# Optimization experiments

Hardware: AMD Instinct MI355X
Metric: run time of the kernel (lower is better)

The kernel has to match this reference:

```python
import jax, jax.numpy as jnp
import numpy as np

NUM_EMBEDDINGS = 1024
EMBEDDING_DIM = 64
BETA = 0.25  # commitment_cost


def setup_inputs() -> dict:
    key = jax.random.key(0)
    k1, k2 = jax.random.split(key)
    z = jax.random.normal(k1, (32, EMBEDDING_DIM, 32, 32), dtype=jnp.float32)
    embedding = jax.random.normal(k2, (NUM_EMBEDDINGS, EMBEDDING_DIM), dtype=jnp.float32)
    return {"z": z, "embedding": embedding}


def reference(z, embedding):
    B, D, H, W = z.shape
    beta = jnp.asarray(BETA, z.dtype)
    # [B, D, H, W] -> [B*H*W, D]
    z_flat = jnp.transpose(z, (0, 2, 3, 1)).reshape(-1, D)
    # squared L2 distances to each code: ||z||^2 - 2 z.e^T + ||e||^2  -> [N, E]
    dist = (
        jnp.sum(z_flat * z_flat, axis=1, keepdims=True)
        - 2.0 * (z_flat @ embedding.T)
        + jnp.sum(embedding * embedding, axis=1)
    )
    encoding_indices = jnp.argmin(dist, axis=1)  # [N]
    # direct gather instead of one-hot matmul (same math)
    quantized = embedding[encoding_indices]  # [N, D]
    quantized = jnp.transpose(quantized.reshape(B, H, W, D), (0, 3, 1, 2))
    commitment_loss = beta * jnp.mean(
        (jax.lax.stop_gradient(z) - quantized) ** 2
    )
    codebook_loss = jnp.mean((z - jax.lax.stop_gradient(quantized)) ** 2)
    loss = commitment_loss + codebook_loss
    # straight-through estimator
    quantized_st = z + jax.lax.stop_gradient(quantized - z)
    return (quantized_st, loss, encoding_indices)
```

## Files before the change

### kernel.cpp

```cpp
#include <hip/hip_runtime.h>

typedef __attribute__((ext_vector_type(8))) short short8;
typedef __attribute__((ext_vector_type(4))) float f32x4;
typedef unsigned int uint32;

#define QOUT 2097152

__device__ __forceinline__ unsigned short f2bf(float f){
  uint32 u = __float_as_uint(f);
  return (unsigned short)((u + 0x7FFFu + ((u >> 16) & 1u)) >> 16);
}
__device__ __forceinline__ float bf2f(unsigned short h){
  return __uint_as_float(((uint32)h) << 16);
}
__device__ __forceinline__ uint32 med3u(uint32 a, uint32 b, uint32 c){
  uint32 d;
  asm("v_med3_u32 %0, %1, %2, %3" : "=v"(d) : "v"(a), "v"(b), "v"(c));
  return d;
}

__global__ void vq_prep(const float* __restrict__ emb, unsigned char* __restrict__ ebg,
                        float* __restrict__ nrm64, int* __restrict__ cnt){
  int u = blockIdx.x * 256 + threadIdx.x;
  if (u == 0) *cnt = 0;
  int C = u >> 3, oct = u & 7;
  const float4* e4 = reinterpret_cast<const float4*>(emb) + C * 16 + oct * 2;
  float4 v0 = e4[0], v1 = e4[1];
  float vv[8] = {v0.x, v0.y, v0.z, v0.w, v1.x, v1.y, v1.z, v1.w};
  float s = 0.f;
  short8 H, L;
#pragma unroll
  for (int j = 0; j < 8; ++j){
    float v = vv[j];
    s = fmaf(v, v, s);
    unsigned short hs = f2bf(v);
    unsigned short ls = f2bf(v - bf2f(hs));
    H[j] = (short)hs; L[j] = (short)ls;
  }
  int ng = C >> 4, c15 = C & 15, kf = oct >> 2, gg = oct & 3;
  unsigned char* base = ebg + ng * 4096 + kf * 2048 + (gg * 16 + c15) * 16;
  *reinterpret_cast<short8*>(base) = H;
  *reinterpret_cast<short8*>(base + 1024) = L;
#pragma unroll
  for (int d = 1; d < 8; d <<= 1) s += __shfl_xor(s, d);
  if (oct == 0) nrm64[C] = 0.5f * s + 128.0f;
}

__global__ __launch_bounds__(512, 4) void vq_main(
    const float* __restrict__ z, const float* __restrict__ emb,
    const unsigned char* __restrict__ ebg, const float* __restrict__ nrm64,
    float* __restrict__ out, float* __restrict__ partial, int* __restrict__ cnt)
{
  __shared__ float zf[64 * 68];
  __shared__ float nrmlds[1024];
  __shared__ uint32 mg[64][4][3];
  __shared__ uint32 cand[64][3];
  __shared__ int kidx[64];
  __shared__ int flagrow[64];
  __shared__ int nflag;
  __shared__ float werr[8];
  __shared__ float red[256];
  __shared__ int isLast;

  const int t = threadIdx.x;
  const int bi = blockIdx.x;
  const int n0 = bi * 64;
  const int b = n0 >> 10;
  const int hw0 = n0 & 1023;
  const int w = t >> 6, lane = t & 63;
  const int wm = w >> 2, wn = w & 3;
  const int l15 = lane & 15, g = lane >> 4;

#pragma unroll
  for (int i = 0; i < 2; ++i) nrmlds[i * 512 + t] = nrm64[i * 512 + t];
  if (t == 0) nflag = 0;

#pragma unroll
  for (int k = 0; k < 8; ++k){
    int li = k * 512 + t;
    int d = li >> 6, j = li & 63;
    zf[j * 68 + d] = z[((b * 64 + d) << 10) + hw0 + j];
  }
  __syncthreads();

  short8 ah[2][2], al[2][2];
#pragma unroll
  for (int mf = 0; mf < 2; ++mf)
#pragma unroll
    for (int kf = 0; kf < 2; ++kf){
      int row = wm * 32 + mf * 16 + l15;
      int base = row * 68 + kf * 32 + g * 8;
      float4 q0 = *reinterpret_cast<float4*>(&zf[base]);
      float4 q1 = *reinterpret_cast<float4*>(&zf[base + 4]);
      float vv[8] = {q0.x,q0.y,q0.z,q0.w,q1.x,q1.y,q1.z,q1.w};
#pragma unroll
      for (int j = 0; j < 8; ++j){
        float v = -vv[j];
        unsigned short hs = f2bf(v);
        unsigned short ls = f2bf(v - bf2f(hs));
        ah[mf][kf][j] = (short)hs;
        al[mf][kf][j] = (short)ls;
      }
    }

  uint32 u0[8], u1[8], u2[8];
#pragma unroll
  for (int s = 0; s < 8; ++s){ u0[s] = 0xFFFFFFFFu; u1[s] = 0xFFFFFFFFu; u2[s] = 0xFFFFFFFFu; }

  const unsigned char* pbase = ebg + (wn << 16) + (lane << 4);
#pragma unroll
  for (int i = 0; i < 16; ++i){
    const unsigned char* p = pbase + (i << 12);
    short8 bh0 = *reinterpret_cast<const short8*>(p);
    short8 bl0 = *reinterpret_cast<const short8*>(p + 1024);
    short8 bh1 = *reinterpret_cast<const short8*>(p + 2048);
    short8 bl1 = *reinterpret_cast<const short8*>(p + 3072);
    int code = ((wn * 16 + i) << 4) + l15;
    float nv = nrmlds[code];
    f32x4 a0 = {nv, nv, nv, nv};
    f32x4 a1 = {nv, nv, nv, nv};
    a0 = __builtin_amdgcn_mfma_f32_16x16x32_bf16(ah[0][0], bh0, a0, 0,0,0);
    a0 = __builtin_amdgcn_mfma_f32_16x16x32_bf16(ah[0][1], bh1, a0, 0,0,0);
    a0 = __builtin_amdgcn_mfma_f32_16x16x32_bf16(al[0][0], bh0, a0, 0,0,0);
    a0 = __builtin_amdgcn_mfma_f32_16x16x32_bf16(al[0][1], bh1, a0, 0,0,0);
    a0 = __builtin_amdgcn_mfma_f32_16x16x32_bf16(ah[0][0], bl0, a0, 0,0,0);
    a0 = __builtin_amdgcn_mfma_f32_16x16x32_bf16(ah[0][1], bl1, a0, 0,0,0);
    a1 = __builtin_amdgcn_mfma_f32_16x16x32_bf16(ah[1][0], bh0, a1, 0,0,0);
    a1 = __builtin_amdgcn_mfma_f32_16x16x32_bf16(ah[1][1], bh1, a1, 0,0,0);
    a1 = __builtin_amdgcn_mfma_f32_16x16x32_bf16(al[1][0], bh0, a1, 0,0,0);
    a1 = __builtin_amdgcn_mfma_f32_16x16x32_bf16(al[1][1], bh1, a1, 0,0,0);
    a1 = __builtin_amdgcn_mfma_f32_16x16x32_bf16(ah[1][0], bl0, a1, 0,0,0);
    a1 = __builtin_amdgcn_mfma_f32_16x16x32_bf16(ah[1][1], bl1, a1, 0,0,0);
    uint32 kb = (uint32)code;
#pragma unroll
    for (int r = 0; r < 4; ++r){
      uint32 k0v = (__float_as_uint(a0[r]) & 0xFFFFFC00u) | kb;
      u2[r] = med3u(k0v, u1[r], u2[r]);
      u1[r] = med3u(k0v, u0[r], u1[r]);
      u0[r] = u0[r] < k0v ? u0[r] : k0v;
      uint32 k1v = (__float_as_uint(a1[r]) & 0xFFFFFC00u) | kb;
      u2[4+r] = med3u(k1v, u1[4+r], u2[4+r]);
      u1[4+r] = med3u(k1v, u0[4+r], u1[4+r]);
      u0[4+r] = u0[4+r] < k1v ? u0[4+r] : k1v;
    }
  }

#pragma unroll
  for (int dm = 1; dm < 16; dm <<= 1){
#pragma unroll
    for (int s = 0; s < 8; ++s){
      uint32 x0 = (uint32)__shfl_xor((int)u0[s], dm);
      uint32 x1 = (uint32)__shfl_xor((int)u1[s], dm);
      uint32 x2 = (uint32)__shfl_xor((int)u2[s], dm);
      u2[s] = med3u(x0, u1[s], u2[s]); u1[s] = med3u(x0, u0[s], u1[s]); u0[s] = u0[s] < x0 ? u0[s] : x0;
      u2[s] = med3u(x1, u1[s], u2[s]); u1[s] = med3u(x1, u0[s], u1[s]); u0[s] = u0[s] < x1 ? u0[s] : x1;
      u2[s] = med3u(x2, u1[s], u2[s]); u1[s] = med3u(x2, u0[s], u1[s]); u0[s] = u0[s] < x2 ? u0[s] : x2;
    }
  }
  if (l15 == 0){
#pragma unroll
    for (int mf = 0; mf < 2; ++mf)
#pragma unroll
      for (int r = 0; r < 4; ++r){
        int lr = wm * 32 + mf * 16 + g * 4 + r;
        int s = mf * 4 + r;
        mg[lr][wn][0] = u0[s]; mg[lr][wn][1] = u1[s]; mg[lr][wn][2] = u2[s];
      }
  }
  __syncthreads();

  if (t < 64){
    uint32 a0k = mg[t][0][0], a1k = mg[t][0][1], a2k = mg[t][0][2];
#pragma unroll
    for (int v = 1; v < 4; ++v)
#pragma unroll
      for (int j2 = 0; j2 < 3; ++j2){
        uint32 x = mg[t][v][j2];
        a2k = med3u(x, a1k, a2k); a1k = med3u(x, a0k, a1k); a0k = a0k < x ? a0k : x;
      }
    kidx[t] = (int)(a0k & 1023u);
    cand[t][0] = a0k; cand[t][1] = a1k; cand[t][2] = a2k;
    float d0 = __uint_as_float(a0k & 0xFFFFFC00u);
    float d1 = __uint_as_float(a1k & 0xFFFFFC00u);
    if (d1 - d0 < 0.0625f){
      int pos = atomicAdd(&nflag, 1);
      flagrow[pos] = t;
    }
  }
  __syncthreads();

  {
    int nf = nflag;
    int cidx = lane >> 4, q = lane & 15;
    for (int n = w; n < nf; n += 8){
      int row = flagrow[n];
      double acc = 0.0;
      if (cidx < 3){
        int k = (int)(cand[row][cidx] & 1023u);
        float4 ev = *reinterpret_cast<const float4*>(emb + k * 64 + q * 4);
        float4 zv = *reinterpret_cast<const float4*>(&zf[row * 68 + q * 4]);
        double d0v = (double)zv.x - (double)ev.x;
        double d1v = (double)zv.y - (double)ev.y;
        double d2v = (double)zv.z - (double)ev.z;
        double d3v = (double)zv.w - (double)ev.w;
        acc = d0v*d0v + d1v*d1v + d2v*d2v + d3v*d3v;
      }
#pragma unroll
      for (int dx = 1; dx < 16; dx <<= 1) acc += __shfl_xor(acc, dx);
      double s0 = __shfl(acc, 0);
      double s1 = __shfl(acc, 16);
      double s2 = __shfl(acc, 32);
      if (lane == 0){
        int k0 = (int)(cand[row][0] & 1023u);
        int k1 = (int)(cand[row][1] & 1023u);
        int k2 = (int)(cand[row][2] & 1023u);
        int bk = k0; double bs = s0;
        if (s1 < bs || (s1 == bs && k1 < bk)) { bs = s1; bk = k1; }
        if (s2 < bs || (s2 == bs && k2 < bk)) { bs = s2; bk = k2; }
        kidx[row] = bk;
      }
    }
  }
  __syncthreads();

  {
    int row = t & 63, dp = t >> 6;
    int k = kidx[row];
    const float4* e4p = reinterpret_cast<const float4*>(emb + k * 64 + dp * 8);
    float4 ev0 = e4p[0], ev1 = e4p[1];
    float evf[8] = {ev0.x,ev0.y,ev0.z,ev0.w, ev1.x,ev1.y,ev1.z,ev1.w};
    float* ob = out + (b << 16) + hw0 + row;
    float err = 0.f;
#pragma unroll
    for (int dd = 0; dd < 8; ++dd){
      int d = dp * 8 + dd;
      float zv = zf[row * 68 + d];
      float qv = evf[dd];
      ob[d << 10] = qv;
      float df = zv - qv;
      err = fmaf(df, df, err);
    }
    if (dp == 0) out[QOUT + 1 + n0 + row] = (float)k;
#pragma unroll
    for (int dx = 1; dx < 64; dx <<= 1) err += __shfl_xor(err, dx);
    if (lane == 0) werr[w] = err;
  }
  __syncthreads();
  if (t == 0){
    partial[bi] = ((werr[0] + werr[1]) + (werr[2] + werr[3]))
                + ((werr[4] + werr[5]) + (werr[6] + werr[7]));
    __threadfence();
    int pos = atomicAdd(cnt, 1);
    isLast = (pos == 511) ? 1 : 0;
  }
  __syncthreads();

  if (isLast){
    __threadfence();
    if (t < 256){
      const volatile float* vp = partial;
      red[t] = vp[t] + vp[t + 256];
    }
    __syncthreads();
    for (int ww = 128; ww > 0; ww >>= 1){
      if (t < ww) red[t] += red[t + ww];
      __syncthreads();
    }
    if (t == 0) out[QOUT] = 1.25f * red[0] * (1.0f / 2097152.0f);
  }
}

extern "C" void kernel_launch(void* const* d_in, const int* in_sizes, int n_in,
                              void* d_out, int out_size, void* d_ws, size_t ws_size,
                              hipStream_t stream) {
  const float* z   = (const float*)d_in[0];
  const float* emb = (const float*)d_in[1];
  float* out = (float*)d_out;
  unsigned char* ebg = (unsigned char*)d_ws;
  float* nrm64   = (float*)(ebg + 262144);
  float* partial = nrm64 + 1024;
  int*   cnt     = (int*)(partial + 512);

  vq_prep <<<32,  256, 0, stream>>>(emb, ebg, nrm64, cnt);
  vq_main <<<512, 512, 0, stream>>>(z, emb, ebg, nrm64, out, partial, cnt);
}
```

Baseline: 45.70 us.

## Split codebook search across four blocks per row tile with separate finalize kernel

```diff
diff --git a/kernel.cpp b/kernel.cpp
--- a/kernel.cpp
+++ b/kernel.cpp
@@ -46,34 +46,25 @@
   if (oct == 0) nrm64[C] = 0.5f * s + 128.0f;
 }
 
-__global__ __launch_bounds__(512, 4) void vq_main(
-    const float* __restrict__ z, const float* __restrict__ emb,
-    const unsigned char* __restrict__ ebg, const float* __restrict__ nrm64,
-    float* __restrict__ out, float* __restrict__ partial, int* __restrict__ cnt)
+__global__ __launch_bounds__(512, 6) void vq_part(
+    const float* __restrict__ z, const unsigned char* __restrict__ ebg,
+    const float* __restrict__ nrm64, uint32* __restrict__ part)
 {
   __shared__ float zf[64 * 68];
-  __shared__ float nrmlds[1024];
+  __shared__ float nrmlds[256];
   __shared__ uint32 mg[64][4][3];
-  __shared__ uint32 cand[64][3];
-  __shared__ int kidx[64];
-  __shared__ int flagrow[64];
-  __shared__ int nflag;
-  __shared__ float werr[8];
-  __shared__ float red[256];
-  __shared__ int isLast;
 
   const int t = threadIdx.x;
   const int bi = blockIdx.x;
-  const int n0 = bi * 64;
+  const int rt = bi >> 2, q = bi & 3;
+  const int n0 = rt * 64;
   const int b = n0 >> 10;
   const int hw0 = n0 & 1023;
   const int w = t >> 6, lane = t & 63;
   const int wm = w >> 2, wn = w & 3;
   const int l15 = lane & 15, g = lane >> 4;
 
-#pragma unroll
-  for (int i = 0; i < 2; ++i) nrmlds[i * 512 + t] = nrm64[i * 512 + t];
-  if (t == 0) nflag = 0;
+  if (t < 256) nrmlds[t] = nrm64[q * 256 + t];
 
 #pragma unroll
   for (int k = 0; k < 8; ++k){
@@ -107,16 +98,17 @@
 #pragma unroll
   for (int s = 0; s < 8; ++s){ u0[s] = 0xFFFFFFFFu; u1[s] = 0xFFFFFFFFu; u2[s] = 0xFFFFFFFFu; }
 
-  const unsigned char* pbase = ebg + (wn << 16) + (lane << 4);
-#pragma unroll
-  for (int i = 0; i < 16; ++i){
+  const int ng0 = q * 16 + wn * 4;
+  const unsigned char* pbase = ebg + (ng0 << 12) + (lane << 4);
+#pragma unroll
+  for (int i = 0; i < 4; ++i){
     const unsigned char* p = pbase + (i << 12);
     short8 bh0 = *reinterpret_cast<const short8*>(p);
     short8 bl0 = *reinterpret_cast<const short8*>(p + 1024);
     short8 bh1 = *reinterpret_cast<const short8*>(p + 2048);
     short8 bl1 = *reinterpret_cast<const short8*>(p + 3072);
-    int code = ((wn * 16 + i) << 4) + l15;
-    float nv = nrmlds[code];
+    int code = ((ng0 + i) << 4) + l15;
+    float nv = nrmlds[((wn * 4 + i) << 4) + l15];
     f32x4 a0 = {nv, nv, nv, nv};
     f32x4 a1 = {nv, nv, nv, nv};
     a0 = __builtin_amdgcn_mfma_f32_16x16x32_bf16(ah[0][0], bh0, a0, 0,0,0);
@@ -178,6 +170,54 @@
         uint32 x = mg[t][v][j2];
         a2k = med3u(x, a1k, a2k); a1k = med3u(x, a0k, a1k); a0k = a0k < x ? a0k : x;
       }
+    uint32* pp = part + (((uint32)bi * 64u + (uint32)t) * 3u);
+    pp[0] = a0k; pp[1] = a1k; pp[2] = a2k;
+  }
+}
+
+__global__ __launch_bounds__(256, 2) void vq_fin(
+    const float* __restrict__ z, const float* __restrict__ emb,
+    const uint32* __restrict__ part, float* __restrict__ out,
+    float* __restrict__ partial, int* __restrict__ cnt)
+{
+  __shared__ float zf[64 * 68];
+  __shared__ uint32 cand[64][3];
+  __shared__ int kidx[64];
+  __shared__ int flagrow[64];
+  __shared__ int nflag;
+  __shared__ float werr[4];
+  __shared__ float red[256];
+  __shared__ int isLast;
+
+  const int t = threadIdx.x;
+  const int bi = blockIdx.x;
+  const int n0 = bi * 64;
+  const int b = n0 >> 10;
+  const int hw0 = n0 & 1023;
+  const int w = t >> 6, lane = t & 63;
+
+  if (t == 0) nflag = 0;
+
+#pragma unroll
+  for (int k = 0; k < 16; ++k){
+    int li = k * 256 + t;
+    int d = li >> 6, j = li & 63;
+    zf[j * 68 + d] = z[((b * 64 + d) << 10) + hw0 + j];
+  }
+  __syncthreads();
+
+  if (t < 64){
+    const uint32* p0 = part + (((uint32)(bi * 4 + 0) * 64u + (uint32)t) * 3u);
+    uint32 a0k = p0[0], a1k = p0[1], a2k = p0[2];
+#pragma unroll
+    for (int qq = 1; qq < 4; ++qq){
+      const uint32* pq = part + (((uint32)(bi * 4 + qq) * 64u + (uint32)t) * 3u);
+#pragma unroll
+      for (int j2 = 0; j2 < 3; ++j2){
+        uint32 x = pq[j2];
+        a2k = med3u(x, a1k, a2k); a1k = med3u(x, a0k, a1k); a0k = a0k < x ? a0k : x;
+      }
+    }
     kidx[t] = (int)(a0k & 1023u);
     cand[t][0] = a0k; cand[t][1] = a1k; cand[t][2] = a2k;
     float d0 = __uint_as_float(a0k & 0xFFFFFC00u);
@@ -191,14 +231,14 @@
 
   {
     int nf = nflag;
-    int cidx = lane >> 4, q = lane & 15;
-    for (int n = w; n < nf; n += 8){
+    int cidx = lane >> 4, qd = lane & 15;
+    for (int n = w; n < nf; n += 4){
       int row = flagrow[n];
       double acc = 0.0;
       if (cidx < 3){
         int k = (int)(cand[row][cidx] & 1023u);
-        float4 ev = *reinterpret_cast<const float4*>(emb + k * 64 + q * 4);
-        float4 zv = *reinterpret_cast<const float4*>(&zf[row * 68 + q * 4]);
+        float4 ev = *reinterpret_cast<const float4*>(emb + k * 64 + qd * 4);
+        float4 zv = *reinterpret_cast<const float4*>(&zf[row * 68 + qd * 4]);
         double d0v = (double)zv.x - (double)ev.x;
         double d1v = (double)zv.y - (double)ev.y;
         double d2v = (double)zv.z - (double)ev.z;
@@ -226,14 +266,15 @@
   {
     int row = t & 63, dp = t >> 6;
     int k = kidx[row];
-    const float4* e4p = reinterpret_cast<const float4*>(emb + k * 64 + dp * 8);
-    float4 ev0 = e4p[0], ev1 = e4p[1];
-    float evf[8] = {ev0.x,ev0.y,ev0.z,ev0.w, ev1.x,ev1.y,ev1.z,ev1.w};
+    const float4* e4p = reinterpret_cast<const float4*>(emb + k * 64 + dp * 16);
+    float4 ev0 = e4p[0], ev1 = e4p[1], ev2 = e4p[2], ev3 = e4p[3];
+    float evf[16] = {ev0.x,ev0.y,ev0.z,ev0.w, ev1.x,ev1.y,ev1.z,ev1.w,
+                     ev2.x,ev2.y,ev2.z,ev2.w, ev3.x,ev3.y,ev3.z,ev3.w};
     float* ob = out + (b << 16) + hw0 + row;
     float err = 0.f;
 #pragma unroll
-    for (int dd = 0; dd < 8; ++dd){
-      int d = dp * 8 + dd;
+    for (int dd = 0; dd < 16; ++dd){
+      int d = dp * 16 + dd;
       float zv = zf[row * 68 + d];
       float qv = evf[dd];
       ob[d << 10] = qv;
@@ -247,8 +288,7 @@
   }
   __syncthreads();
   if (t == 0){
-    partial[bi] = ((werr[0] + werr[1]) + (werr[2] + werr[3]))
-                + ((werr[4] + werr[5]) + (werr[6] + werr[7]));
+    partial[bi] = (werr[0] + werr[1]) + (werr[2] + werr[3]);
     __threadfence();
     int pos = atomicAdd(cnt, 1);
     isLast = (pos == 511) ? 1 : 0;
@@ -257,10 +297,8 @@
 
   if (isLast){
     __threadfence();
-    if (t < 256){
-      const volatile float* vp = partial;
-      red[t] = vp[t] + vp[t + 256];
-    }
+    const volatile float* vp = partial;
+    red[t] = vp[t] + vp[t + 256];
     __syncthreads();
     for (int ww = 128; ww > 0; ww >>= 1){
       if (t < ww) red[t] += red[t + ww];
@@ -277,10 +315,12 @@
   const float* emb = (const float*)d_in[1];
   float* out = (float*)d_out;
   unsigned char* ebg = (unsigned char*)d_ws;
-  float* nrm64   = (float*)(ebg + 262144);
-  float* partial = nrm64 + 1024;
-  int*   cnt     = (int*)(partial + 512);
-
-  vq_prep <<<32,  256, 0, stream>>>(emb, ebg, nrm64, cnt);
-  vq_main <<<512, 512, 0, stream>>>(z, emb, ebg, nrm64, out, partial, cnt);
-}
+  float*  nrm64   = (float*)(ebg + 262144);
+  uint32* part    = (uint32*)(ebg + 266240);
+  float*  partial = (float*)(ebg + 266240 + 1572864);
+  int*    cnt     = (int*)(ebg + 266240 + 1572864 + 2048);
+
+  vq_prep <<<32,   256, 0, stream>>>(emb, ebg, nrm64, cnt);
+  vq_part <<<2048, 512, 0, stream>>>(z, ebg, nrm64, part);
+  vq_fin  <<<512,  256, 0, stream>>>(z, emb, part, out, partial, cnt);
+}
```

Result: slower. 112.4 us (+145.9%).
